# Performance work log

Measured on AMD Instinct MI355X. Metric: run time of the kernel, lower is better.

Reference implementation:

```python
import jax, jax.numpy as jnp
import numpy as np

B, S, I, H = 32, 512, 1024, 1024


def _rnn_pass(x, W_ih, W_hh, b_ih, b_hh):
    # x: [B,S,I]; vanilla tanh RNN, h0 = 0. Precompute input projection once.
    xp = jnp.einsum('bsi,hi->bsh', x, W_ih) + b_ih + b_hh  # [B,S,H]
    h0 = jnp.zeros((x.shape[0], W_hh.shape[0]), dtype=x.dtype)

    def step(h, xp_t):
        h_new = jnp.tanh(xp_t + h @ W_hh.T)
        return h_new, h_new

    _, outs = jax.lax.scan(step, h0, jnp.swapaxes(xp, 0, 1))  # [S,B,H]
    return jnp.swapaxes(outs, 0, 1)  # [B,S,H]


def setup_inputs() -> dict:
    key = jax.random.key(0)
    ks = jax.random.split(key, 9)
    scale_i = 1.0 / np.sqrt(I)
    scale_h = 1.0 / np.sqrt(H)
    return {
        'x': jax.random.normal(ks[0], (B, S, I), dtype=jnp.float32),
        'W_ih_f': jax.random.normal(ks[1], (H, I), dtype=jnp.float32) * scale_i,
        'W_hh_f': jax.random.normal(ks[2], (H, H), dtype=jnp.float32) * scale_h,
        'b_ih_f': jax.random.normal(ks[3], (H,), dtype=jnp.float32) * scale_h,
        'b_hh_f': jax.random.normal(ks[4], (H,), dtype=jnp.float32) * scale_h,
        'W_ih_b': jax.random.normal(ks[5], (H, I), dtype=jnp.float32) * scale_i,
        'W_hh_b': jax.random.normal(ks[6], (H, H), dtype=jnp.float32) * scale_h,
        'b_ih_b': jax.random.normal(ks[7], (H,), dtype=jnp.float32) * scale_h,
        'b_hh_b': jax.random.normal(ks[8], (H,), dtype=jnp.float32) * scale_h,
    }


def reference(x, W_ih_f, W_hh_f, b_ih_f, b_hh_f, W_ih_b, W_hh_b, b_ih_b, b_hh_b):
    fwd = _rnn_pass(x, W_ih_f, W_hh_f, b_ih_f, b_hh_f)              # [B,S,H]
    bwd = _rnn_pass(x[:, ::-1, :], W_ih_b, W_hh_b, b_ih_b, b_hh_b)  # reversed seq
    bwd = bwd[:, ::-1, :]                                           # flip back
    return jnp.concatenate([fwd, bwd], axis=-1)  # [B,S,2H]
```

## Files before the change

### kernel.cpp

```cpp
#include <hip/hip_runtime.h>

typedef _Float16 half8  __attribute__((ext_vector_type(8)));
typedef _Float16 half4v __attribute__((ext_vector_type(4)));
typedef float    floatx4 __attribute__((ext_vector_type(4)));
typedef unsigned long long u64;

#define B_ 32
#define S_ 512
#define I_ 1024
#define H_ 1024
#define M_TOT (B_ * S_)

__global__ void cvt_f32_f16(const float* __restrict__ src, _Float16* __restrict__ dst, long n) {
  long i = ((long)blockIdx.x * blockDim.x + threadIdx.x) * 4;
  const long stride = (long)gridDim.x * blockDim.x * 4;
  for (; i < n; i += stride) {
    floatx4 v = *(const floatx4*)(src + i);
    half4v h = {(_Float16)v[0], (_Float16)v[1], (_Float16)v[2], (_Float16)v[3]};
    *(half4v*)(dst + i) = h;
  }
}

__global__ void bias_sum_kernel(const float* __restrict__ bihf, const float* __restrict__ bhhf,
                                const float* __restrict__ bihb, const float* __restrict__ bhhb,
                                float* __restrict__ bias, unsigned int* __restrict__ ctrs) {
  int i = blockIdx.x * blockDim.x + threadIdx.x;
  if (i < 1024) {
    __hip_atomic_store(ctrs + i, 0u, __ATOMIC_RELAXED, __HIP_MEMORY_SCOPE_AGENT);
  }
  if (i < H_) {
    bias[i]      = bihf[i] + bhhf[i];
    bias[H_ + i] = bihb[i] + bhhb[i];
  }
}

__global__ void __launch_bounds__(256) gemm_xp_kernel(
    const _Float16* __restrict__ A,
    const _Float16* __restrict__ W,
    const float*    __restrict__ bias,
    float*          __restrict__ out)
{
  __shared__ _Float16 alds[128 * 32];
  __shared__ _Float16 blds[128 * 32];

  const int dir = blockIdx.z;
  const int m0  = blockIdx.y * 128;
  const int n0  = blockIdx.x * 128;
  const int tid  = threadIdx.x;
  const int lane = tid & 63;
  const int wv   = tid >> 6;
  const int wm   = wv >> 1, wn = wv & 1;
  const int lrow = lane & 15;
  const int lkg  = lane >> 4;

  const _Float16* Wd = W + (long)dir * H_ * I_;

  floatx4 acc[4][4] = {};

  const int srow = tid >> 1;
  const int sseg = tid & 1;

  for (int kt = 0; kt < 32; ++kt) {
    __syncthreads();
    {
      const _Float16* srcA = A  + (long)(m0 + srow) * I_ + kt * 32 + sseg * 16;
      const _Float16* srcB = Wd + (long)(n0 + srow) * I_ + kt * 32 + sseg * 16;
      half8 a0 = *(const half8*)(srcA);
      half8 a1 = *(const half8*)(srcA + 8);
      half8 b0 = *(const half8*)(srcB);
      half8 b1 = *(const half8*)(srcB + 8);
      const int sw = (srow & 7) << 4;
      const int base = srow * 64 + sseg * 32;
      *(half8*)((char*)alds + ((base     ) ^ sw)) = a0;
      *(half8*)((char*)alds + ((base + 16) ^ sw)) = a1;
      *(half8*)((char*)blds + ((base     ) ^ sw)) = b0;
      *(half8*)((char*)blds + ((base + 16) ^ sw)) = b1;
    }
    __syncthreads();

    half8 af[4], bf[4];
#pragma unroll
    for (int mt = 0; mt < 4; ++mt) {
      int r = wm * 64 + mt * 16 + lrow;
      int byte = (r * 64 + lkg * 16) ^ ((r & 7) << 4);
      af[mt] = *(const half8*)((const char*)alds + byte);
    }
#pragma unroll
    for (int ntt = 0; ntt < 4; ++ntt) {
      int r = wn * 64 + ntt * 16 + lrow;
      int byte = (r * 64 + lkg * 16) ^ ((r & 7) << 4);
      bf[ntt] = *(const half8*)((const char*)blds + byte);
    }
#pragma unroll
    for (int mt = 0; mt < 4; ++mt)
#pragma unroll
      for (int ntt = 0; ntt < 4; ++ntt)
        acc[mt][ntt] = __builtin_amdgcn_mfma_f32_16x16x32_f16(af[mt], bf[ntt], acc[mt][ntt], 0, 0, 0);
  }

#pragma unroll
  for (int mt = 0; mt < 4; ++mt) {
    int mrow = m0 + wm * 64 + mt * 16 + lkg * 4;
#pragma unroll
    for (int ntt = 0; ntt < 4; ++ntt) {
      int n = n0 + wn * 64 + ntt * 16 + lrow;
      float bv = bias[dir * H_ + n];
#pragma unroll
      for (int v = 0; v < 4; ++v) {
        out[(long)(mrow + v) * (2 * H_) + dir * H_ + n] = acc[mt][ntt][v] + bv;
      }
    }
  }
}

__global__ void __launch_bounds__(256, 1) scan_kernel(
    const float* __restrict__ Whh_f,
    const float* __restrict__ Whh_b,
    float*       __restrict__ out,
    _Float16*    __restrict__ hbuf,
    unsigned int* __restrict__ ctrs)
{
  __shared__ _Float16 wlds[32 * 1024];
  __shared__ floatx4  redlds[2 * 4 * 64];

  const int w     = blockIdx.x;
  const int dir   = w >> 5;
  const int rb    = w & 31;
  const int rows0 = rb * 32;
  const float* Whh = dir ? Whh_b : Whh_f;
  const int tid = threadIdx.x;

  for (int idx = tid; idx < 32 * 128; idx += 256) {
    const int r  = idx >> 7;
    const int kg = idx & 127;
    const float* src = Whh + (long)(rows0 + r) * H_ + kg * 8;
    floatx4 v0 = *(const floatx4*)(src);
    floatx4 v1 = *(const floatx4*)(src + 4);
    half8 h = {(_Float16)v0[0], (_Float16)v0[1], (_Float16)v0[2], (_Float16)v0[3],
               (_Float16)v1[0], (_Float16)v1[1], (_Float16)v1[2], (_Float16)v1[3]};
    const int byte = (r * 2048 + kg * 16) ^ ((r & 7) << 4);
    *(half8*)((char*)wlds + byte) = h;
  }

  const int lane = tid & 63;
  const int wv   = tid >> 6;
  const int nt   = wv & 1;
  const int kh   = wv >> 1;
  const int lrow = lane & 15;
  const int lkg  = lane >> 4;
  const int b_idx = nt * 16 + lrow;
  const int kbase = kh * 512;
  const int r0    = rows0 + kh * 16 + lkg * 4;
  const int asw   = (lrow & 7) << 4;
  const int abase0 = lrow * 2048 + kbase * 2;
  const int abase1 = (16 + lrow) * 2048 + kbase * 2;

  unsigned int* sig  = ctrs + (((dir * 2 + nt) * 2 + kh) * 4 + (rb >> 3)) * 32;
  unsigned int* pbas = ctrs + ((dir * 2 + nt) * 8) * 32;

  {
    u64* pz = (u64*)(hbuf + ((long)(0 * 2 + dir) * B_ + b_idx) * H_ + r0);
    __hip_atomic_store(pz, (u64)0, __ATOMIC_RELAXED, __HIP_MEMORY_SCOPE_AGENT);
  }
  asm volatile("s_waitcnt vmcnt(0)" ::: "memory");
  __syncthreads();
  if (lane == 0)
    __hip_atomic_fetch_add(sig, 1u, __ATOMIC_RELAXED, __HIP_MEMORY_SCOPE_AGENT);

  long o_nxt = ((long)b_idx * S_ + (dir ? (S_ - 1) : 0)) * (2 * H_) + dir * H_ + r0;
  floatx4 xp_n = *(const floatx4*)(out + o_nxt);

#pragma unroll 1
  for (int t = 0; t < S_; ++t) {
    const int p = t & 1;

    {
      const unsigned int tgt = 8u * (unsigned)(t + 1);
      for (;;) {
        unsigned int v = tgt;
        if (lane < 8)
          v = __hip_atomic_load(pbas + lane * 32, __ATOMIC_RELAXED, __HIP_MEMORY_SCOPE_AGENT);
        if (__all((int)(v >= tgt))) break;
        __builtin_amdgcn_s_sleep(1);
      }
    }

    const _Float16* hp = hbuf + ((long)(p * 2 + dir) * B_ + b_idx) * H_ + kbase + lkg * 8;
    half8 hr[16];
#pragma unroll
    for (int kt = 0; kt < 16; ++kt)
      asm volatile("global_load_dwordx4 %0, %1, off offset:%2 sc1"
                   : "=v"(hr[kt]) : "v"(hp), "i"(kt * 64) : "memory");
    asm volatile("s_waitcnt vmcnt(0)" ::: "memory");
    __builtin_amdgcn_sched_barrier(0);

    floatx4 a0 = {}, a1 = {};
#pragma unroll
    for (int kt = 0; kt < 16; ++kt) {
      const int koff = kt * 64 + lkg * 16;
      half8 wa = *(const half8*)((const char*)wlds + ((abase0 + koff) ^ asw));
      half8 wb = *(const half8*)((const char*)wlds + ((abase1 + koff) ^ asw));
      a0 = __builtin_amdgcn_mfma_f32_16x16x32_f16(wa, hr[kt], a0, 0, 0, 0);
      a1 = __builtin_amdgcn_mfma_f32_16x16x32_f16(wb, hr[kt], a1, 0, 0, 0);
    }

    redlds[((p * 2 + (1 - kh)) * 2 + nt) * 64 + lane] = kh ? a0 : a1;
    __syncthreads();
    floatx4 tot = (kh ? a1 : a0) + redlds[((p * 2 + kh) * 2 + nt) * 64 + lane];

    const long o = o_nxt;
    const floatx4 xpv = xp_n;
    floatx4 hv;
#pragma unroll
    for (int v = 0; v < 4; ++v) {
      float z = tot[v] + xpv[v];
      hv[v] = 1.f - 2.f / (__expf(2.f * z) + 1.f);
    }

    if (t + 1 < S_) {
      union { half4v h; u64 u; } hh;
      hh.h = half4v{(_Float16)hv[0], (_Float16)hv[1], (_Float16)hv[2], (_Float16)hv[3]};
      u64* dst = (u64*)(hbuf + ((long)((1 - p) * 2 + dir) * B_ + b_idx) * H_ + r0);
      __hip_atomic_store(dst, hh.u, __ATOMIC_RELAXED, __HIP_MEMORY_SCOPE_AGENT);
      asm volatile("s_waitcnt vmcnt(0)" ::: "memory");
      if (lane == 0)
        __hip_atomic_fetch_add(sig, 1u, __ATOMIC_RELAXED, __HIP_MEMORY_SCOPE_AGENT);
    }

    *(floatx4*)(out + o) = hv;
    if (t + 1 < S_) {
      const int sidx1 = dir ? (S_ - 2 - t) : (t + 1);
      o_nxt = ((long)b_idx * S_ + sidx1) * (2 * H_) + dir * H_ + r0;
      xp_n = *(const floatx4*)(out + o_nxt);
    }
  }
}

extern "C" void kernel_launch(void* const* d_in, const int* in_sizes, int n_in,
                              void* d_out, int out_size, void* d_ws, size_t ws_size,
                              hipStream_t stream) {
  const float* x    = (const float*)d_in[0];
  const float* Wihf = (const float*)d_in[1];
  const float* Whhf = (const float*)d_in[2];
  const float* bihf = (const float*)d_in[3];
  const float* bhhf = (const float*)d_in[4];
  const float* Wihb = (const float*)d_in[5];
  const float* Whhb = (const float*)d_in[6];
  const float* bihb = (const float*)d_in[7];
  const float* bhhb = (const float*)d_in[8];
  float* out = (float*)d_out;

  char* ws = (char*)d_ws;
  _Float16*     x16  = (_Float16*)ws;
  _Float16*     w16  = (_Float16*)(ws + 33554432u);
  float*        bias = (float*)   (ws + 33554432u + 4194304u);
  _Float16*     hbuf = (_Float16*)(ws + 37756928u);
  unsigned int* ctrs = (unsigned int*)(ws + 38019072u);

  cvt_f32_f16<<<4096, 256, 0, stream>>>(x, x16, (long)M_TOT * I_);
  cvt_f32_f16<<<1024, 256, 0, stream>>>(Wihf, w16, (long)H_ * I_);
  cvt_f32_f16<<<1024, 256, 0, stream>>>(Wihb, w16 + (long)H_ * I_, (long)H_ * I_);
  bias_sum_kernel<<<4, 256, 0, stream>>>(bihf, bhhf, bihb, bhhb, bias, ctrs);

  dim3 g(H_ / 128, M_TOT / 128, 2);
  gemm_xp_kernel<<<g, 256, 0, stream>>>(x16, w16, bias, out);

  void* args[] = {(void*)&Whhf, (void*)&Whhb, (void*)&out, (void*)&hbuf, (void*)&ctrs};
  (void)hipLaunchCooperativeKernel((void*)scan_kernel, dim3(64), dim3(256),
                                   args, 0, stream);
}
```

Measured before the change: 2.254 ms.

## Halve scan grid so each block owns 64 hidden rows

```diff
diff --git a/kernel.cpp b/kernel.cpp
--- a/kernel.cpp
+++ b/kernel.cpp
@@ -120,17 +120,17 @@
     _Float16*    __restrict__ hbuf,
     unsigned int* __restrict__ ctrs)
 {
-  __shared__ _Float16 wlds[32 * 1024];
-  __shared__ floatx4  redlds[2 * 4 * 64];
+  __shared__ _Float16 wlds[64 * 1024];
+  __shared__ floatx4  redlds[2 * 4 * 2 * 64];
 
   const int w     = blockIdx.x;
-  const int dir   = w >> 5;
-  const int rb    = w & 31;
-  const int rows0 = rb * 32;
+  const int dir   = w >> 4;
+  const int rb    = w & 15;
+  const int rows0 = rb * 64;
   const float* Whh = dir ? Whh_b : Whh_f;
   const int tid = threadIdx.x;
 
-  for (int idx = tid; idx < 32 * 128; idx += 256) {
+  for (int idx = tid; idx < 64 * 128; idx += 256) {
     const int r  = idx >> 7;
     const int kg = idx & 127;
     const float* src = Whh + (long)(rows0 + r) * H_ + kg * 8;
@@ -150,25 +150,33 @@
   const int lkg  = lane >> 4;
   const int b_idx = nt * 16 + lrow;
   const int kbase = kh * 512;
-  const int r0    = rows0 + kh * 16 + lkg * 4;
   const int asw   = (lrow & 7) << 4;
-  const int abase0 = lrow * 2048 + kbase * 2;
-  const int abase1 = (16 + lrow) * 2048 + kbase * 2;
-
-  unsigned int* sig  = ctrs + (((dir * 2 + nt) * 2 + kh) * 4 + (rb >> 3)) * 32;
-  unsigned int* pbas = ctrs + ((dir * 2 + nt) * 8) * 32;
+  const int abase0 = (lrow     ) * 2048 + kbase * 2;
+  const int abase1 = (lrow + 16) * 2048 + kbase * 2;
+  const int abase2 = (lrow + 32) * 2048 + kbase * 2;
+  const int abase3 = (lrow + 48) * 2048 + kbase * 2;
+  const int r0a = rows0 + (kh * 2    ) * 16 + lkg * 4;
+  const int r0b = rows0 + (kh * 2 + 1) * 16 + lkg * 4;
+
+  unsigned int* sig  = ctrs + ((((dir * 2 + nt) * 2 + kh) * 2) + (rb >> 3)) * 32;
+  unsigned int* pbas = ctrs + ((dir * 2 + nt) * 4) * 32;
 
   {
-    u64* pz = (u64*)(hbuf + ((long)(0 * 2 + dir) * B_ + b_idx) * H_ + r0);
-    __hip_atomic_store(pz, (u64)0, __ATOMIC_RELAXED, __HIP_MEMORY_SCOPE_AGENT);
+    u64* pza = (u64*)(hbuf + ((long)(0 * 2 + dir) * B_ + b_idx) * H_ + r0a);
+    u64* pzb = (u64*)(hbuf + ((long)(0 * 2 + dir) * B_ + b_idx) * H_ + r0b);
+    __hip_atomic_store(pza, (u64)0, __ATOMIC_RELAXED, __HIP_MEMORY_SCOPE_AGENT);
+    __hip_atomic_store(pzb, (u64)0, __ATOMIC_RELAXED, __HIP_MEMORY_SCOPE_AGENT);
   }
   asm volatile("s_waitcnt vmcnt(0)" ::: "memory");
   __syncthreads();
   if (lane == 0)
     __hip_atomic_fetch_add(sig, 1u, __ATOMIC_RELAXED, __HIP_MEMORY_SCOPE_AGENT);
 
-  long o_nxt = ((long)b_idx * S_ + (dir ? (S_ - 1) : 0)) * (2 * H_) + dir * H_ + r0;
-  floatx4 xp_n = *(const floatx4*)(out + o_nxt);
+  const int s0 = dir ? (S_ - 1) : 0;
+  long oa_n = ((long)b_idx * S_ + s0) * (2 * H_) + dir * H_ + r0a;
+  long ob_n = ((long)b_idx * S_ + s0) * (2 * H_) + dir * H_ + r0b;
+  floatx4 xpa_n = *(const floatx4*)(out + oa_n);
+  floatx4 xpb_n = *(const floatx4*)(out + ob_n);
 
 #pragma unroll 1
   for (int t = 0; t < S_; ++t) {
@@ -178,7 +186,7 @@
       const unsigned int tgt = 8u * (unsigned)(t + 1);
       for (;;) {
         unsigned int v = tgt;
-        if (lane < 8)
+        if (lane < 4)
           v = __hip_atomic_load(pbas + lane * 32, __ATOMIC_RELAXED, __HIP_MEMORY_SCOPE_AGENT);
         if (__all((int)(v >= tgt))) break;
         __builtin_amdgcn_s_sleep(1);
@@ -194,44 +202,64 @@
     asm volatile("s_waitcnt vmcnt(0)" ::: "memory");
     __builtin_amdgcn_sched_barrier(0);
 
-    floatx4 a0 = {}, a1 = {};
+    floatx4 a0 = {}, a1 = {}, a2 = {}, a3 = {};
 #pragma unroll
     for (int kt = 0; kt < 16; ++kt) {
       const int koff = kt * 64 + lkg * 16;
-      half8 wa = *(const half8*)((const char*)wlds + ((abase0 + koff) ^ asw));
-      half8 wb = *(const half8*)((const char*)wlds + ((abase1 + koff) ^ asw));
-      a0 = __builtin_amdgcn_mfma_f32_16x16x32_f16(wa, hr[kt], a0, 0, 0, 0);
-      a1 = __builtin_amdgcn_mfma_f32_16x16x32_f16(wb, hr[kt], a1, 0, 0, 0);
-    }
-
-    redlds[((p * 2 + (1 - kh)) * 2 + nt) * 64 + lane] = kh ? a0 : a1;
+      half8 w0 = *(const half8*)((const char*)wlds + ((abase0 + koff) ^ asw));
+      half8 w1 = *(const half8*)((const char*)wlds + ((abase1 + koff) ^ asw));
+      half8 w2 = *(const half8*)((const char*)wlds + ((abase2 + koff) ^ asw));
+      half8 w3 = *(const half8*)((const char*)wlds + ((abase3 + koff) ^ asw));
+      a0 = __builtin_amdgcn_mfma_f32_16x16x32_f16(w0, hr[kt], a0, 0, 0, 0);
+      a1 = __builtin_amdgcn_mfma_f32_16x16x32_f16(w1, hr[kt], a1, 0, 0, 0);
+      a2 = __builtin_amdgcn_mfma_f32_16x16x32_f16(w2, hr[kt], a2, 0, 0, 0);
+      a3 = __builtin_amdgcn_mfma_f32_16x16x32_f16(w3, hr[kt], a3, 0, 0, 0);
+    }
+
+    {
+      const int shipA = (1 - kh) * 2;
+      floatx4 sA = kh ? a0 : a2;
+      floatx4 sB = kh ? a1 : a3;
+      redlds[((p * 4 + shipA    ) * 2 + nt) * 64 + lane] = sA;
+      redlds[((p * 4 + shipA + 1) * 2 + nt) * 64 + lane] = sB;
+    }
     __syncthreads();
-    floatx4 tot = (kh ? a1 : a0) + redlds[((p * 2 + kh) * 2 + nt) * 64 + lane];
-
-    const long o = o_nxt;
-    const floatx4 xpv = xp_n;
-    floatx4 hv;
+    const int ownA = kh * 2;
+    floatx4 totA = (kh ? a2 : a0) + redlds[((p * 4 + ownA    ) * 2 + nt) * 64 + lane];
+    floatx4 totB = (kh ? a3 : a1) + redlds[((p * 4 + ownA + 1) * 2 + nt) * 64 + lane];
+
+    const long oa = oa_n, ob = ob_n;
+    const floatx4 xpa = xpa_n, xpb = xpb_n;
+    floatx4 hva, hvb;
 #pragma unroll
     for (int v = 0; v < 4; ++v) {
-      float z = tot[v] + xpv[v];
-      hv[v] = 1.f - 2.f / (__expf(2.f * z) + 1.f);
+      float za = totA[v] + xpa[v];
+      float zb = totB[v] + xpb[v];
+      hva[v] = 1.f - 2.f / (__expf(2.f * za) + 1.f);
+      hvb[v] = 1.f - 2.f / (__expf(2.f * zb) + 1.f);
     }
 
     if (t + 1 < S_) {
-      union { half4v h; u64 u; } hh;
-      hh.h = half4v{(_Float16)hv[0], (_Float16)hv[1], (_Float16)hv[2], (_Float16)hv[3]};
-      u64* dst = (u64*)(hbuf + ((long)((1 - p) * 2 + dir) * B_ + b_idx) * H_ + r0);
-      __hip_atomic_store(dst, hh.u, __ATOMIC_RELAXED, __HIP_MEMORY_SCOPE_AGENT);
+      union { half4v h; u64 u; } ha, hb;
+      ha.h = half4v{(_Float16)hva[0], (_Float16)hva[1], (_Float16)hva[2], (_Float16)hva[3]};
+      hb.h = half4v{(_Float16)hvb[0], (_Float16)hvb[1], (_Float16)hvb[2], (_Float16)hvb[3]};
+      u64* da = (u64*)(hbuf + ((long)((1 - p) * 2 + dir) * B_ + b_idx) * H_ + r0a);
+      u64* db = (u64*)(hbuf + ((long)((1 - p) * 2 + dir) * B_ + b_idx) * H_ + r0b);
+      __hip_atomic_store(da, ha.u, __ATOMIC_RELAXED, __HIP_MEMORY_SCOPE_AGENT);
+      __hip_atomic_store(db, hb.u, __ATOMIC_RELAXED, __HIP_MEMORY_SCOPE_AGENT);
       asm volatile("s_waitcnt vmcnt(0)" ::: "memory");
       if (lane == 0)
         __hip_atomic_fetch_add(sig, 1u, __ATOMIC_RELAXED, __HIP_MEMORY_SCOPE_AGENT);
     }
 
-    *(floatx4*)(out + o) = hv;
+    *(floatx4*)(out + oa) = hva;
+    *(floatx4*)(out + ob) = hvb;
     if (t + 1 < S_) {
       const int sidx1 = dir ? (S_ - 2 - t) : (t + 1);
-      o_nxt = ((long)b_idx * S_ + sidx1) * (2 * H_) + dir * H_ + r0;
-      xp_n = *(const floatx4*)(out + o_nxt);
+      oa_n = ((long)b_idx * S_ + sidx1) * (2 * H_) + dir * H_ + r0a;
+      ob_n = ((long)b_idx * S_ + sidx1) * (2 * H_) + dir * H_ + r0b;
+      xpa_n = *(const floatx4*)(out + oa_n);
+      xpb_n = *(const floatx4*)(out + ob_n);
     }
   }
 }
@@ -266,6 +294,6 @@
   gemm_xp_kernel<<<g, 256, 0, stream>>>(x16, w16, bias, out);
 
   void* args[] = {(void*)&Whhf, (void*)&Whhb, (void*)&out, (void*)&hbuf, (void*)&ctrs};
-  (void)hipLaunchCooperativeKernel((void*)scan_kernel, dim3(64), dim3(256),
+  (void)hipLaunchCooperativeKernel((void*)scan_kernel, dim3(32), dim3(256),
                                    args, 0, stream);
 }
```

Result: slower. 2.815 ms (+24.9%).

## Replace counter barrier with parity-tagged fp16 hidden-state ring buffer

Applied to the files above, without the earlier changes.

```diff
diff --git a/kernel.cpp b/kernel.cpp
--- a/kernel.cpp
+++ b/kernel.cpp
@@ -23,15 +23,19 @@
 
 __global__ void bias_sum_kernel(const float* __restrict__ bihf, const float* __restrict__ bhhf,
                                 const float* __restrict__ bihb, const float* __restrict__ bhhb,
-                                float* __restrict__ bias, unsigned int* __restrict__ ctrs) {
+                                float* __restrict__ bias) {
   int i = blockIdx.x * blockDim.x + threadIdx.x;
-  if (i < 1024) {
-    __hip_atomic_store(ctrs + i, 0u, __ATOMIC_RELAXED, __HIP_MEMORY_SCOPE_AGENT);
-  }
   if (i < H_) {
     bias[i]      = bihf[i] + bhhf[i];
     bias[H_ + i] = bihb[i] + bhhb[i];
   }
+}
+
+__global__ void init_ring(unsigned int* __restrict__ hq) {
+  const int i = blockIdx.x * blockDim.x + threadIdx.x;
+  unsigned int v = 0u;
+  if (i >= 32768) v = (i < 65536) ? 0x00020002u : 0x00010001u;
+  __hip_atomic_store(hq + i, v, __ATOMIC_RELAXED, __HIP_MEMORY_SCOPE_AGENT);
 }
 
 __global__ void __launch_bounds__(256) gemm_xp_kernel(
@@ -117,8 +121,7 @@
     const float* __restrict__ Whh_f,
     const float* __restrict__ Whh_b,
     float*       __restrict__ out,
-    _Float16*    __restrict__ hbuf,
-    unsigned int* __restrict__ ctrs)
+    _Float16*    __restrict__ hbuf)
 {
   __shared__ _Float16 wlds[32 * 1024];
   __shared__ floatx4  redlds[2 * 4 * 64];
@@ -155,43 +158,38 @@
   const int abase0 = lrow * 2048 + kbase * 2;
   const int abase1 = (16 + lrow) * 2048 + kbase * 2;
 
-  unsigned int* sig  = ctrs + (((dir * 2 + nt) * 2 + kh) * 4 + (rb >> 3)) * 32;
-  unsigned int* pbas = ctrs + ((dir * 2 + nt) * 8) * 32;
-
-  {
-    u64* pz = (u64*)(hbuf + ((long)(0 * 2 + dir) * B_ + b_idx) * H_ + r0);
-    __hip_atomic_store(pz, (u64)0, __ATOMIC_RELAXED, __HIP_MEMORY_SCOPE_AGENT);
-  }
-  asm volatile("s_waitcnt vmcnt(0)" ::: "memory");
+  const long hstride = (long)2 * B_ * H_;
+
   __syncthreads();
-  if (lane == 0)
-    __hip_atomic_fetch_add(sig, 1u, __ATOMIC_RELAXED, __HIP_MEMORY_SCOPE_AGENT);
 
   long o_nxt = ((long)b_idx * S_ + (dir ? (S_ - 1) : 0)) * (2 * H_) + dir * H_ + r0;
   floatx4 xp_n = *(const floatx4*)(out + o_nxt);
+
+  int s_in = 0;
 
 #pragma unroll 1
   for (int t = 0; t < S_; ++t) {
     const int p = t & 1;
-
-    {
-      const unsigned int tgt = 8u * (unsigned)(t + 1);
-      for (;;) {
-        unsigned int v = tgt;
-        if (lane < 8)
-          v = __hip_atomic_load(pbas + lane * 32, __ATOMIC_RELAXED, __HIP_MEMORY_SCOPE_AGENT);
-        if (__all((int)(v >= tgt))) break;
-        __builtin_amdgcn_s_sleep(1);
+    const int s_out = (s_in == 2) ? 0 : (s_in + 1);
+
+    const _Float16* hp = hbuf + (s_in * hstride) + ((long)dir * B_ + b_idx) * H_ + kbase + lkg * 8;
+    const unsigned int rep = (unsigned)(t & 1) * 0x00010001u;
+    half8 hr[16];
+    for (;;) {
+#pragma unroll
+      for (int kt = 0; kt < 16; ++kt)
+        asm volatile("global_load_dwordx4 %0, %1, off offset:%2 sc1"
+                     : "=v"(hr[kt]) : "v"(hp), "i"(kt * 64) : "memory");
+      asm volatile("s_waitcnt vmcnt(0)" ::: "memory");
+      unsigned int bad = 0;
+#pragma unroll
+      for (int kt = 0; kt < 16; ++kt) {
+        union { half8 h; unsigned int u[4]; } c; c.h = hr[kt];
+        bad |= ((c.u[0] ^ rep) | (c.u[1] ^ rep) | (c.u[2] ^ rep) | (c.u[3] ^ rep))
+               & 0x00010001u;
       }
-    }
-
-    const _Float16* hp = hbuf + ((long)(p * 2 + dir) * B_ + b_idx) * H_ + kbase + lkg * 8;
-    half8 hr[16];
-#pragma unroll
-    for (int kt = 0; kt < 16; ++kt)
-      asm volatile("global_load_dwordx4 %0, %1, off offset:%2 sc1"
-                   : "=v"(hr[kt]) : "v"(hp), "i"(kt * 64) : "memory");
-    asm volatile("s_waitcnt vmcnt(0)" ::: "memory");
+      if (!__any(bad != 0)) break;
+    }
     __builtin_amdgcn_sched_barrier(0);
 
     floatx4 a0 = {}, a1 = {};
@@ -218,13 +216,13 @@
     }
 
     if (t + 1 < S_) {
-      union { half4v h; u64 u; } hh;
+      union { half4v h; u64 u; unsigned int w2[2]; } hh;
       hh.h = half4v{(_Float16)hv[0], (_Float16)hv[1], (_Float16)hv[2], (_Float16)hv[3]};
-      u64* dst = (u64*)(hbuf + ((long)((1 - p) * 2 + dir) * B_ + b_idx) * H_ + r0);
+      const unsigned int eo = (unsigned)((t + 1) & 1) * 0x00010001u;
+      hh.w2[0] = (hh.w2[0] & ~0x00010001u) | eo;
+      hh.w2[1] = (hh.w2[1] & ~0x00010001u) | eo;
+      u64* dst = (u64*)(hbuf + (s_out * hstride) + ((long)dir * B_ + b_idx) * H_ + r0);
       __hip_atomic_store(dst, hh.u, __ATOMIC_RELAXED, __HIP_MEMORY_SCOPE_AGENT);
-      asm volatile("s_waitcnt vmcnt(0)" ::: "memory");
-      if (lane == 0)
-        __hip_atomic_fetch_add(sig, 1u, __ATOMIC_RELAXED, __HIP_MEMORY_SCOPE_AGENT);
     }
 
     *(floatx4*)(out + o) = hv;
@@ -233,6 +231,7 @@
       o_nxt = ((long)b_idx * S_ + sidx1) * (2 * H_) + dir * H_ + r0;
       xp_n = *(const floatx4*)(out + o_nxt);
     }
+    s_in = s_out;
   }
 }
 
@@ -255,17 +254,17 @@
   _Float16*     w16  = (_Float16*)(ws + 33554432u);
   float*        bias = (float*)   (ws + 33554432u + 4194304u);
   _Float16*     hbuf = (_Float16*)(ws + 37756928u);
-  unsigned int* ctrs = (unsigned int*)(ws + 38019072u);
 
   cvt_f32_f16<<<4096, 256, 0, stream>>>(x, x16, (long)M_TOT * I_);
   cvt_f32_f16<<<1024, 256, 0, stream>>>(Wihf, w16, (long)H_ * I_);
   cvt_f32_f16<<<1024, 256, 0, stream>>>(Wihb, w16 + (long)H_ * I_, (long)H_ * I_);
-  bias_sum_kernel<<<4, 256, 0, stream>>>(bihf, bhhf, bihb, bhhb, bias, ctrs);
+  bias_sum_kernel<<<4, 256, 0, stream>>>(bihf, bhhf, bihb, bhhb, bias);
+  init_ring<<<384, 256, 0, stream>>>((unsigned int*)hbuf);
 
   dim3 g(H_ / 128, M_TOT / 128, 2);
   gemm_xp_kernel<<<g, 256, 0, stream>>>(x16, w16, bias, out);
 
-  void* args[] = {(void*)&Whhf, (void*)&Whhb, (void*)&out, (void*)&hbuf, (void*)&ctrs};
+  void* args[] = {(void*)&Whhf, (void*)&Whhb, (void*)&out, (void*)&hbuf};
   (void)hipLaunchCooperativeKernel((void*)scan_kernel, dim3(64), dim3(256),
                                    args, 0, stream);
 }
```

Result: no change. 2.211 ms (-1.9%).
